# Performance work log

Hardware: AMD Instinct MI355X
Metric: run time of the kernel (lower is better)

Reference implementation:

```python
import jax, jax.numpy as jnp
import numpy as np

BATCH, IN_DIM, HID, STATES = 4096, 256, 512, 16

def setup_inputs() -> dict:
    key = jax.random.key(0)
    k1, k2, k3 = jax.random.split(key, 3)
    x = jax.random.normal(k1, (BATCH, IN_DIM), dtype=jnp.float32)
    h_quantum = jax.random.normal(k2, (BATCH, HID, STATES), dtype=jnp.float32)
    # param initialized with normal(0.1) stddev in the original
    W_quantum = jax.random.normal(k3, (IN_DIM, HID, STATES), dtype=jnp.float32) * 0.1
    return {"x": x, "h_quantum": h_quantum, "W_quantum": W_quantum}

def reference(x, h_quantum, W_quantum):
    # Fused equivalent of the per-state loop: one batched contraction
    # input_contrib[b,h,s] = sum_i x[b,i] * W[i,h,s]
    input_contrib = jnp.einsum('bi,ihs->bhs', x, W_quantum)
    new_quantum_state = jnp.tanh(input_contrib + h_quantum * 0.9)
    output = jnp.mean(new_quantum_state, axis=-1)  # [B, HID]
    return (output, new_quantum_state)
```

## Files before the change

kernel.cpp:

```cpp
#include <hip/hip_runtime.h>

#define BATCH  4096
#define IN_DIM 256
#define HID    512
#define NCOL   8192

#define BM 128
#define BN 64

typedef __attribute__((ext_vector_type(8))) short bf16x8;
typedef __attribute__((ext_vector_type(4))) float f32x4;
typedef __attribute__((ext_vector_type(4))) float fvec4;

typedef __attribute__((address_space(1))) const unsigned as1_uint;
typedef __attribute__((address_space(3))) unsigned       as3_uint;

__device__ __forceinline__ uint pack_hi(float f0, float f1) {
    return __builtin_amdgcn_perm(__builtin_bit_cast(uint, f1),
                                 __builtin_bit_cast(uint, f0), 0x07060302u);
}
__device__ __forceinline__ float hi_part(float f) {
    return __builtin_bit_cast(float, __builtin_bit_cast(uint, f) & 0xFFFF0000u);
}
__device__ __forceinline__ float tanh_fast(float x) {
    float e = __builtin_amdgcn_exp2f(x * 2.8853900817779268f);
    float r = __builtin_amdgcn_rcpf(e + 1.0f);
    return __builtin_fmaf(-2.0f, r, 1.0f);
}
__device__ __forceinline__ void split8(const float* f, uint4& h, uint4& l) {
    h.x = pack_hi(f[0], f[1]); h.y = pack_hi(f[2], f[3]);
    h.z = pack_hi(f[4], f[5]); h.w = pack_hi(f[6], f[7]);
    l.x = pack_hi(f[0] - hi_part(f[0]), f[1] - hi_part(f[1]));
    l.y = pack_hi(f[2] - hi_part(f[2]), f[3] - hi_part(f[3]));
    l.z = pack_hi(f[4] - hi_part(f[4]), f[5] - hi_part(f[5]));
    l.w = pack_hi(f[6] - hi_part(f[6]), f[7] - hi_part(f[7]));
}

#define W_ELEMS  2097152
#define X_ELEMS  1048576
#define WS_NEED  (12u * 1024u * 1024u)

__global__ __launch_bounds__(256) void prep_w_kernel(
    const float* __restrict__ W, ushort* __restrict__ whi, ushort* __restrict__ wlo)
{
    const int n    = blockIdx.x * 256 + threadIdx.x;
    const int koct = blockIdx.y;
    float f[8];
    #pragma unroll
    for (int j = 0; j < 8; ++j)
        f[j] = __builtin_nontemporal_load(&W[(size_t)(koct * 8 + j) * NCOL + n]);
    uint4 h, l;
    split8(f, h, l);
    const size_t o = ((size_t)((n >> 4) * 32 + koct) * 16 + (n & 15)) * 8;
    *(uint4*)(whi + o) = h;
    *(uint4*)(wlo + o) = l;
}

__global__ __launch_bounds__(256) void prep_x_kernel(
    const float* __restrict__ x, ushort* __restrict__ xhi, ushort* __restrict__ xlo)
{
    const int b    = blockIdx.x * 256 + threadIdx.x;
    const int koct = blockIdx.y;
    float f[8];
    fvec4 v0 = __builtin_nontemporal_load((const fvec4*)&x[(size_t)b * IN_DIM + koct * 8]);
    fvec4 v1 = __builtin_nontemporal_load((const fvec4*)&x[(size_t)b * IN_DIM + koct * 8 + 4]);
    f[0] = v0.x; f[1] = v0.y; f[2] = v0.z; f[3] = v0.w;
    f[4] = v1.x; f[5] = v1.y; f[6] = v1.z; f[7] = v1.w;
    uint4 h, l;
    split8(f, h, l);
    const size_t o = ((size_t)((b >> 4) * 32 + koct) * 16 + (b & 15)) * 8;
    *(uint4*)(xhi + o) = h;
    *(uint4*)(xlo + o) = l;
}

__global__ __launch_bounds__(256, 3) void mqc_main_kernel(
    const ushort* __restrict__ xhi, const ushort* __restrict__ xlo,
    const ushort* __restrict__ whi, const ushort* __restrict__ wlo,
    const float* __restrict__ hq,
    float* __restrict__ out_mean, float* __restrict__ out_new)
{
    __shared__ ushort sBh[8192], sBl[8192];

    const int t     = threadIdx.x;
    const int lane  = t & 63;
    const int w     = t >> 6;
    const int lquad = lane >> 4;
    const int l16   = lane & 15;

    const int wgid = blockIdx.x;
    const int xcd  = wgid & 7;
    const int q    = wgid >> 3;
    const int rowg = (xcd << 2) | (q & 3);
    const int colg = q >> 2;
    const int row0 = rowg * BM;
    const int col0 = colg * BN;
    const int btile0 = (row0 >> 4) + w * 2;
    const int ntile0 = col0 >> 4;

    f32x4 acc[2][4] = {};

    #define STAGE(KOCT0) {                                                          \
        _Pragma("unroll")                                                           \
        for (int itc = 0; itc < 8; ++itc) {                                         \
            const int c  = itc * 4 + w;                                             \
            const int nt = (c >> 2) & 3;                                            \
            const int kl = (c & 3) * 4 + (lane >> 4);                               \
            const ushort* srcp = ((c >> 4) ? wlo : whi)                             \
                + ((size_t)(ntile0 + nt) * 32 + (KOCT0) + kl) * 128 + (lane & 15) * 8; \
            ushort* dstp = ((c >> 4) ? sBl : sBh) + nt * 2048 + (c & 3) * 512;      \
            __builtin_amdgcn_global_load_lds((as1_uint*)srcp, (as3_uint*)dstp,      \
                                             16, 0, 0);                             \
        }                                                                           \
    }

    #define APREF(AH, AL, KOCT0, SL0) {                                             \
        _Pragma("unroll")                                                           \
        for (int s = 0; s < 2; ++s) {                                               \
            const int koct = (KOCT0) + ((SL0) + s) * 4 + lquad;                     \
            _Pragma("unroll")                                                       \
            for (int mi = 0; mi < 2; ++mi) {                                        \
                const size_t o = ((size_t)(btile0 + mi) * 32 + koct) * 128 + l16 * 8; \
                AH[s][mi] = *(const bf16x8*)(xhi + o);                              \
                AL[s][mi] = *(const bf16x8*)(xlo + o);                              \
            }                                                                       \
        }                                                                           \
    }

    #define KSTEP2(AH, AL, SL0) {                                                   \
        _Pragma("unroll")                                                           \
        for (int s = 0; s < 2; ++s) {                                               \
            const int bidx = (((SL0) + s) * 4 + lquad) * 128 + l16 * 8;             \
            bf16x8 bH[4], bL[4];                                                    \
            _Pragma("unroll")                                                       \
            for (int ni = 0; ni < 4; ++ni) {                                        \
                bH[ni] = *(const bf16x8*)(sBh + ni * 2048 + bidx);                  \
                bL[ni] = *(const bf16x8*)(sBl + ni * 2048 + bidx);                  \
            }                                                                       \
            _Pragma("unroll")                                                       \
            for (int mi = 0; mi < 2; ++mi)                                          \
                _Pragma("unroll")                                                   \
                for (int ni = 0; ni < 4; ++ni)                                      \
                    acc[mi][ni] = __builtin_amdgcn_mfma_f32_16x16x32_bf16(bH[ni], AH[s][mi], acc[mi][ni], 0, 0, 0); \
            _Pragma("unroll")                                                       \
            for (int mi = 0; mi < 2; ++mi)                                          \
                _Pragma("unroll")                                                   \
                for (int ni = 0; ni < 4; ++ni)                                      \
                    acc[mi][ni] = __builtin_amdgcn_mfma_f32_16x16x32_bf16(bH[ni], AL[s][mi], acc[mi][ni], 0, 0, 0); \
            _Pragma("unroll")                                                       \
            for (int mi = 0; mi < 2; ++mi)                                          \
                _Pragma("unroll")                                                   \
                for (int ni = 0; ni < 4; ++ni)                                      \
                    acc[mi][ni] = __builtin_amdgcn_mfma_f32_16x16x32_bf16(bL[ni], AH[s][mi], acc[mi][ni], 0, 0, 0); \
        }                                                                           \
    }

    bf16x8 AaH[2][2], AaL[2][2], AbH[2][2], AbL[2][2];
    fvec4 hv[2][4];

    STAGE(0);
    APREF(AaH, AaL, 0, 0);
    __syncthreads();
    APREF(AbH, AbL, 0, 2);
    KSTEP2(AaH, AaL, 0);
    KSTEP2(AbH, AbL, 2);
    __syncthreads();
    STAGE(16);
    APREF(AaH, AaL, 16, 0);
    __syncthreads();
    APREF(AbH, AbL, 16, 2);
    KSTEP2(AaH, AaL, 0);
    #pragma unroll
    for (int mi = 0; mi < 2; ++mi) {
        const int b = row0 + w * 32 + mi * 16 + l16;
        #pragma unroll
        for (int ni = 0; ni < 4; ++ni) {
            const int n = col0 + ni * 16 + lquad * 4;
            hv[mi][ni] = *(const fvec4*)&hq[(size_t)b * NCOL + n];
        }
    }
    KSTEP2(AbH, AbL, 2);
    #undef STAGE
    #undef APREF
    #undef KSTEP2

    #pragma unroll
    for (int mi = 0; mi < 2; ++mi) {
        const int b = row0 + w * 32 + mi * 16 + l16;
        #pragma unroll
        for (int ni = 0; ni < 4; ++ni) {
            const int n = col0 + ni * 16 + lquad * 4;
            fvec4 ov;
            ov.x = tanh_fast(__builtin_fmaf(0.9f, hv[mi][ni].x, acc[mi][ni][0]));
            ov.y = tanh_fast(__builtin_fmaf(0.9f, hv[mi][ni].y, acc[mi][ni][1]));
            ov.z = tanh_fast(__builtin_fmaf(0.9f, hv[mi][ni].z, acc[mi][ni][2]));
            ov.w = tanh_fast(__builtin_fmaf(0.9f, hv[mi][ni].w, acc[mi][ni][3]));
            __builtin_nontemporal_store(ov, (fvec4*)&out_new[(size_t)b * NCOL + n]);
            float s = (ov.x + ov.y) + (ov.z + ov.w);
            s += __shfl_xor(s, 16);
            s += __shfl_xor(s, 32);
            if (lquad == 0)
                out_mean[(size_t)b * HID + (col0 >> 4) + ni] = s * 0.0625f;
        }
    }
}

#define BKF 64
__device__ __forceinline__ int swz(int row, int byteoff) {
    return byteoff ^ ((((row & 7) ^ ((row >> 3) & 7))) << 4);
}
__global__ __launch_bounds__(256, 4) void mqc_fallback_kernel(
    const float* __restrict__ x, const float* __restrict__ hq,
    const float* __restrict__ W,
    float* __restrict__ out_mean, float* __restrict__ out_new)
{
    __shared__ char sB[2 * BN * BKF * 2];
    char* const sB_hi = sB;
    char* const sB_lo = sB + BN * BKF * 2;
    const int t = threadIdx.x, lane = t & 63, w = t >> 6;
    const int lquad = lane >> 4, l16 = lane & 15;
    const int row0 = blockIdx.x * BM, col0 = blockIdx.y * BN;
    const int k0 = (t >> 4) * 4, n0 = (t & 15) * 4;
    f32x4 acc[2][4] = {};
    for (int kt = 0; kt < IN_DIM / BKF; ++kt) {
        float4 ax[2][2][2];
        #pragma unroll
        for (int mi = 0; mi < 2; ++mi)
            #pragma unroll
            for (int ks = 0; ks < 2; ++ks) {
                const float* p = &x[(size_t)(row0 + w * 32 + mi * 16 + l16) * IN_DIM
                                    + kt * BKF + ks * 32 + lquad * 8];
                ax[mi][ks][0] = *(const float4*)(p);
                ax[mi][ks][1] = *(const float4*)(p + 4);
            }
        float4 wrow[4];
        #pragma unroll
        for (int r = 0; r < 4; ++r)
            wrow[r] = *(const float4*)(&W[(size_t)(kt * BKF + k0 + r) * NCOL + col0 + n0]);
        #pragma unroll
        for (int c = 0; c < 4; ++c) {
            const float f0 = ((const float*)&wrow[0])[c];
            const float f1 = ((const float*)&wrow[1])[c];
            const float f2 = ((const float*)&wrow[2])[c];
            const float f3 = ((const float*)&wrow[3])[c];
            uint2 hv2, lv2;
            hv2.x = pack_hi(f0, f1); hv2.y = pack_hi(f2, f3);
            lv2.x = pack_hi(f0 - hi_part(f0), f1 - hi_part(f1));
            lv2.y = pack_hi(f2 - hi_part(f2), f3 - hi_part(f3));
            const int off = swz(n0 + c, (n0 + c) * (BKF * 2) + k0 * 2);
            *(uint2*)(sB_hi + off) = hv2;
            *(uint2*)(sB_lo + off) = lv2;
        }
        __syncthreads();
        #pragma unroll
        for (int ks = 0; ks < 2; ++ks) {
            bf16x8 aH[2], aL[2];
            #pragma unroll
            for (int mi = 0; mi < 2; ++mi) {
                uint4 h, l;
                split8((const float*)&ax[mi][ks][0], h, l);
                aH[mi] = __builtin_bit_cast(bf16x8, h);
                aL[mi] = __builtin_bit_cast(bf16x8, l);
            }
            const int kb = ks * 64 + lquad * 16;
            bf16x8 bH[4], bL[4];
            #pragma unroll
            for (int ni = 0; ni < 4; ++ni) {
                const int row = ni * 16 + l16;
                bH[ni] = *(const bf16x8*)(sB_hi + swz(row, row * (BKF * 2) + kb));
            }
            #pragma unroll
            for (int mi = 0; mi < 2; ++mi)
                #pragma unroll
                for (int ni = 0; ni < 4; ++ni)
                    acc[mi][ni] = __builtin_amdgcn_mfma_f32_16x16x32_bf16(bH[ni], aH[mi], acc[mi][ni], 0, 0, 0);
            #pragma unroll
            for (int mi = 0; mi < 2; ++mi)
                #pragma unroll
                for (int ni = 0; ni < 4; ++ni)
                    acc[mi][ni] = __builtin_amdgcn_mfma_f32_16x16x32_bf16(bH[ni], aL[mi], acc[mi][ni], 0, 0, 0);
            #pragma unroll
            for (int ni = 0; ni < 4; ++ni) {
                const int row = ni * 16 + l16;
                bL[ni] = *(const bf16x8*)(sB_lo + swz(row, row * (BKF * 2) + kb));
            }
            #pragma unroll
            for (int mi = 0; mi < 2; ++mi)
                #pragma unroll
                for (int ni = 0; ni < 4; ++ni)
                    acc[mi][ni] = __builtin_amdgcn_mfma_f32_16x16x32_bf16(bL[ni], aH[mi], acc[mi][ni], 0, 0, 0);
        }
        __syncthreads();
    }
    #pragma unroll
    for (int mi = 0; mi < 2; ++mi) {
        const int b = row0 + w * 32 + mi * 16 + l16;
        #pragma unroll
        for (int ni = 0; ni < 4; ++ni) {
            const int n = col0 + ni * 16 + lquad * 4;
            const float4 hv = *(const float4*)(&hq[(size_t)b * NCOL + n]);
            float4 ov;
            ov.x = tanh_fast(__builtin_fmaf(0.9f, hv.x, acc[mi][ni][0]));
            ov.y = tanh_fast(__builtin_fmaf(0.9f, hv.y, acc[mi][ni][1]));
            ov.z = tanh_fast(__builtin_fmaf(0.9f, hv.z, acc[mi][ni][2]));
            ov.w = tanh_fast(__builtin_fmaf(0.9f, hv.w, acc[mi][ni][3]));
            *(float4*)(&out_new[(size_t)b * NCOL + n]) = ov;
            float s = (ov.x + ov.y) + (ov.z + ov.w);
            s += __shfl_xor(s, 16);
            s += __shfl_xor(s, 32);
            if (lquad == 0)
                out_mean[(size_t)b * HID + (col0 >> 4) + ni] = s * 0.0625f;
        }
    }
}

extern "C" void kernel_launch(void* const* d_in, const int* in_sizes, int n_in,
                              void* d_out, int out_size, void* d_ws, size_t ws_size,
                              hipStream_t stream) {
    const float* x  = (const float*)d_in[0];
    const float* hq = (const float*)d_in[1];
    const float* W  = (const float*)d_in[2];

    float* out_mean = (float*)d_out;
    float* out_new  = (float*)d_out + (size_t)BATCH * HID;

    if (ws_size >= WS_NEED) {
        ushort* whi = (ushort*)d_ws;
        ushort* wlo = whi + W_ELEMS;
        ushort* xhi = wlo + W_ELEMS;
        ushort* xlo = xhi + X_ELEMS;
        prep_w_kernel<<<dim3(NCOL / 256, IN_DIM / 8), 256, 0, stream>>>(W, whi, wlo);
        prep_x_kernel<<<dim3(BATCH / 256, IN_DIM / 8), 256, 0, stream>>>(x, xhi, xlo);
        mqc_main_kernel<<<dim3(BATCH * NCOL / (BM * BN)), 256, 0, stream>>>(
            xhi, xlo, whi, wlo, hq, out_mean, out_new);
    } else {
        mqc_fallback_kernel<<<dim3(BATCH / BM, NCOL / BN), 256, 0, stream>>>(
            x, hq, W, out_mean, out_new);
    }
}
```

Before: 93.04 us.

## Process two column tiles per workgroup and overlap epilogue with next tile's MFMAs

Result: slower. 124.4 us (+33.7%).

```diff
diff --git a/kernel.cpp b/kernel.cpp
--- a/kernel.cpp
+++ b/kernel.cpp
@@ -91,22 +91,21 @@
     const int xcd  = wgid & 7;
     const int q    = wgid >> 3;
     const int rowg = (xcd << 2) | (q & 3);
-    const int colg = q >> 2;
+    const int pairg= q >> 2;
     const int row0 = rowg * BM;
-    const int col0 = colg * BN;
+    const int col0 = pairg * 128;
     const int btile0 = (row0 >> 4) + w * 2;
-    const int ntile0 = col0 >> 4;
-
-    f32x4 acc[2][4] = {};
-
-    #define STAGE(KOCT0) {                                                          \
+    const int nt0A  = col0 >> 4;
+    const int nt0B  = nt0A + 4;
+
+    #define STAGE(NT0, KOCT0) {                                                     \
         _Pragma("unroll")                                                           \
         for (int itc = 0; itc < 8; ++itc) {                                         \
             const int c  = itc * 4 + w;                                             \
             const int nt = (c >> 2) & 3;                                            \
             const int kl = (c & 3) * 4 + (lane >> 4);                               \
             const ushort* srcp = ((c >> 4) ? wlo : whi)                             \
-                + ((size_t)(ntile0 + nt) * 32 + (KOCT0) + kl) * 128 + (lane & 15) * 8; \
+                + ((size_t)((NT0) + nt) * 32 + (KOCT0) + kl) * 128 + (lane & 15) * 8; \
             ushort* dstp = ((c >> 4) ? sBl : sBh) + nt * 2048 + (c & 3) * 512;      \
             __builtin_amdgcn_global_load_lds((as1_uint*)srcp, (as3_uint*)dstp,      \
                                              16, 0, 0);                             \
@@ -126,7 +125,7 @@
         }                                                                           \
     }
 
-    #define KSTEP2(AH, AL, SL0) {                                                   \
+    #define KSTEP2(ACC, AH, AL, SL0) {                                              \
         _Pragma("unroll")                                                           \
         for (int s = 0; s < 2; ++s) {                                               \
             const int bidx = (((SL0) + s) * 4 + lquad) * 128 + l16 * 8;             \
@@ -140,68 +139,102 @@
             for (int mi = 0; mi < 2; ++mi)                                          \
                 _Pragma("unroll")                                                   \
                 for (int ni = 0; ni < 4; ++ni)                                      \
-                    acc[mi][ni] = __builtin_amdgcn_mfma_f32_16x16x32_bf16(bH[ni], AH[s][mi], acc[mi][ni], 0, 0, 0); \
+                    ACC[mi][ni] = __builtin_amdgcn_mfma_f32_16x16x32_bf16(bH[ni], AH[s][mi], ACC[mi][ni], 0, 0, 0); \
             _Pragma("unroll")                                                       \
             for (int mi = 0; mi < 2; ++mi)                                          \
                 _Pragma("unroll")                                                   \
                 for (int ni = 0; ni < 4; ++ni)                                      \
-                    acc[mi][ni] = __builtin_amdgcn_mfma_f32_16x16x32_bf16(bH[ni], AL[s][mi], acc[mi][ni], 0, 0, 0); \
+                    ACC[mi][ni] = __builtin_amdgcn_mfma_f32_16x16x32_bf16(bH[ni], AL[s][mi], ACC[mi][ni], 0, 0, 0); \
             _Pragma("unroll")                                                       \
             for (int mi = 0; mi < 2; ++mi)                                          \
                 _Pragma("unroll")                                                   \
                 for (int ni = 0; ni < 4; ++ni)                                      \
-                    acc[mi][ni] = __builtin_amdgcn_mfma_f32_16x16x32_bf16(bL[ni], AH[s][mi], acc[mi][ni], 0, 0, 0); \
-        }                                                                           \
-    }
-
+                    ACC[mi][ni] = __builtin_amdgcn_mfma_f32_16x16x32_bf16(bL[ni], AH[s][mi], ACC[mi][ni], 0, 0, 0); \
+        }                                                                           \
+    }
+
+    #define HVLOAD(HV, COL0T) {                                                     \
+        _Pragma("unroll")                                                           \
+        for (int mi = 0; mi < 2; ++mi) {                                            \
+            const int b = row0 + w * 32 + mi * 16 + l16;                            \
+            _Pragma("unroll")                                                       \
+            for (int ni = 0; ni < 4; ++ni) {                                        \
+                const int n = (COL0T) + ni * 16 + lquad * 4;                        \
+                HV[mi][ni] = *(const fvec4*)&hq[(size_t)b * NCOL + n];              \
+            }                                                                       \
+        }                                                                           \
+    }
+
+    #define EPI_HALF(ACC, HV, COL0T, MI) {                                          \
+        const int b = row0 + w * 32 + (MI) * 16 + l16;                              \
+        _Pragma("unroll")                                                           \
+        for (int ni = 0; ni < 4; ++ni) {                                            \
+            const int n = (COL0T) + ni * 16 + lquad * 4;                            \
+            fvec4 ov;                                                               \
+            ov.x = tanh_fast(__builtin_fmaf(0.9f, HV[MI][ni].x, ACC[MI][ni][0]));   \
+            ov.y = tanh_fast(__builtin_fmaf(0.9f, HV[MI][ni].y, ACC[MI][ni][1]));   \
+            ov.z = tanh_fast(__builtin_fmaf(0.9f, HV[MI][ni].z, ACC[MI][ni][2]));   \
+            ov.w = tanh_fast(__builtin_fmaf(0.9f, HV[MI][ni].w, ACC[MI][ni][3]));   \
+            __builtin_nontemporal_store(ov, (fvec4*)&out_new[(size_t)b * NCOL + n]); \
+            float ssum = (ov.x + ov.y) + (ov.z + ov.w);                             \
+            ssum += __shfl_xor(ssum, 16);                                           \
+            ssum += __shfl_xor(ssum, 32);                                           \
+            if (lquad == 0)                                                         \
+                out_mean[(size_t)b * HID + ((COL0T) >> 4) + ni] = ssum * 0.0625f;   \
+        }                                                                           \
+    }
+
+    f32x4 accA[2][4] = {};
+    f32x4 accB[2][4];
     bf16x8 AaH[2][2], AaL[2][2], AbH[2][2], AbL[2][2];
     fvec4 hv[2][4];
 
-    STAGE(0);
+    STAGE(nt0A, 0);
     APREF(AaH, AaL, 0, 0);
     __syncthreads();
     APREF(AbH, AbL, 0, 2);
-    KSTEP2(AaH, AaL, 0);
-    KSTEP2(AbH, AbL, 2);
-    __syncthreads();
-    STAGE(16);
+    KSTEP2(accA, AaH, AaL, 0);
+    KSTEP2(accA, AbH, AbL, 2);
+    __syncthreads();
+    STAGE(nt0A, 16);
     APREF(AaH, AaL, 16, 0);
     __syncthreads();
     APREF(AbH, AbL, 16, 2);
-    KSTEP2(AaH, AaL, 0);
+    KSTEP2(accA, AaH, AaL, 0);
+    KSTEP2(accA, AbH, AbL, 2);
+    __syncthreads();
+
     #pragma unroll
-    for (int mi = 0; mi < 2; ++mi) {
-        const int b = row0 + w * 32 + mi * 16 + l16;
-        #pragma unroll
-        for (int ni = 0; ni < 4; ++ni) {
-            const int n = col0 + ni * 16 + lquad * 4;
-            hv[mi][ni] = *(const fvec4*)&hq[(size_t)b * NCOL + n];
-        }
-    }
-    KSTEP2(AbH, AbL, 2);
+    for (int mi = 0; mi < 2; ++mi)
+        #pragma unroll
+        for (int ni = 0; ni < 4; ++ni)
+            accB[mi][ni] = (f32x4){0.0f, 0.0f, 0.0f, 0.0f};
+
+    STAGE(nt0B, 0);
+    APREF(AaH, AaL, 0, 0);
+    HVLOAD(hv, col0);
+    __syncthreads();
+    APREF(AbH, AbL, 0, 2);
+    KSTEP2(accB, AaH, AaL, 0);
+    EPI_HALF(accA, hv, col0, 0);
+    KSTEP2(accB, AbH, AbL, 2);
+    __syncthreads();
+    STAGE(nt0B, 16);
+    APREF(AaH, AaL, 16, 0);
+    __syncthreads();
+    APREF(AbH, AbL, 16, 2);
+    KSTEP2(accB, AaH, AaL, 0);
+    EPI_HALF(accA, hv, col0, 1);
+    HVLOAD(hv, col0 + 64);
+    KSTEP2(accB, AbH, AbL, 2);
+    EPI_HALF(accB, hv, col0 + 64, 0);
+    EPI_HALF(accB, hv, col0 + 64, 1);
+
     #undef STAGE
     #undef APREF
     #undef KSTEP2
-
-    #pragma unroll
-    for (int mi = 0; mi < 2; ++mi) {
-        const int b = row0 + w * 32 + mi * 16 + l16;
-        #pragma unroll
-        for (int ni = 0; ni < 4; ++ni) {
-            const int n = col0 + ni * 16 + lquad * 4;
-            fvec4 ov;
-            ov.x = tanh_fast(__builtin_fmaf(0.9f, hv[mi][ni].x, acc[mi][ni][0]));
-            ov.y = tanh_fast(__builtin_fmaf(0.9f, hv[mi][ni].y, acc[mi][ni][1]));
-            ov.z = tanh_fast(__builtin_fmaf(0.9f, hv[mi][ni].z, acc[mi][ni][2]));
-            ov.w = tanh_fast(__builtin_fmaf(0.9f, hv[mi][ni].w, acc[mi][ni][3]));
-            __builtin_nontemporal_store(ov, (fvec4*)&out_new[(size_t)b * NCOL + n]);
-            float s = (ov.x + ov.y) + (ov.z + ov.w);
-            s += __shfl_xor(s, 16);
-            s += __shfl_xor(s, 32);
-            if (lquad == 0)
-                out_mean[(size_t)b * HID + (col0 >> 4) + ni] = s * 0.0625f;
-        }
-    }
+    #undef HVLOAD
+    #undef EPI_HALF
 }
 
 #define BKF 64
@@ -330,7 +363,7 @@
         ushort* xlo = xhi + X_ELEMS;
         prep_w_kernel<<<dim3(NCOL / 256, IN_DIM / 8), 256, 0, stream>>>(W, whi, wlo);
         prep_x_kernel<<<dim3(BATCH / 256, IN_DIM / 8), 256, 0, stream>>>(x, xhi, xlo);
-        mqc_main_kernel<<<dim3(BATCH * NCOL / (BM * BN)), 256, 0, stream>>>(
+        mqc_main_kernel<<<dim3(BATCH * NCOL / (BM * 2 * BN)), 256, 0, stream>>>(
             xhi, xlo, whi, wlo, hq, out_mean, out_new);
     } else {
         mqc_fallback_kernel<<<dim3(BATCH / BM, NCOL / BN), 256, 0, stream>>>(
```
